# Kernel optimization log

Hardware: AMD Instinct MI355X
Metric: run time of the kernel (lower is better)

## Reference

```python
import jax, jax.numpy as jnp
import numpy as np


def setup_inputs() -> dict:
    key = jax.random.key(0)
    ks = jax.random.split(key, 9)
    B, T, D, H = 64, 512, 512, 512
    inp = {
        "x": jax.random.normal(ks[0], (B, T, D), dtype=jnp.float32),
        "W_c": jax.random.normal(ks[1], (D, H), dtype=jnp.float32) * 0.02,
        "W_i": jax.random.normal(ks[2], (D, H), dtype=jnp.float32) * 0.02,
        "W_f": jax.random.normal(ks[3], (D, H), dtype=jnp.float32) * 0.02,
        "W_o": jax.random.normal(ks[4], (D, H), dtype=jnp.float32) * 0.02,
        "U_c": jax.random.normal(ks[5], (H, H), dtype=jnp.float32) * 0.02,
        "U_i": jax.random.normal(ks[6], (H, H), dtype=jnp.float32) * 0.02,
        "U_f": jax.random.normal(ks[7], (H, H), dtype=jnp.float32) * 0.02,
        "U_o": jax.random.normal(ks[8], (H, H), dtype=jnp.float32) * 0.02,
        "b_c": jnp.zeros((H,), dtype=jnp.float32),
        "b_i": jnp.zeros((H,), dtype=jnp.float32),
        "b_f": jnp.zeros((H,), dtype=jnp.float32),
        "b_o": jnp.zeros((H,), dtype=jnp.float32),
    }
    return inp


def reference(x, W_c, W_i, W_f, W_o, U_c, U_i, U_f, U_o, b_c, b_i, b_f, b_o):
    # x: [B, T, D] -> scan over time-major [T, B, D]
    B, T, D = x.shape
    H = W_c.shape[1]
    h0 = jnp.zeros((B, H), dtype=x.dtype)
    c0 = jnp.zeros((B, H), dtype=x.dtype)

    # Precompute input projections for all timesteps (same math, hoisted
    # out of the recurrence since x does not depend on state).
    xt = jnp.transpose(x, (1, 0, 2))  # [T, B, D]
    xa = jnp.einsum('tbd,dh->tbh', xt, W_c) + b_c
    xi = jnp.einsum('tbd,dh->tbh', xt, W_i) + b_i
    xf = jnp.einsum('tbd,dh->tbh', xt, W_f) + b_f
    xo = jnp.einsum('tbd,dh->tbh', xt, W_o) + b_o

    def step(carry, elems):
        h, c = carry
        xa_t, xi_t, xf_t, xo_t = elems
        a = jnp.tanh(xa_t + h @ U_c)
        i = jax.nn.sigmoid(xi_t + h @ U_i)
        f = jax.nn.sigmoid(xf_t + h @ U_f)
        o = jax.nn.sigmoid(xo_t + h @ U_o)
        c_new = i * a + f * c
        h_new = o * jnp.tanh(c_new)
        return (h_new, c_new), h_new

    _, hs = jax.lax.scan(step, (h0, c0), (xa, xi, xf, xo))  # hs: [T, B, H]
    return jnp.transpose(hs, (1, 0, 2))  # return_sequence=True -> [B, T, H]
```

## Files before the change

### kernel.cpp

```cpp
#include <hip/hip_runtime.h>
#include <cstdint>
#include <cstddef>

typedef _Float16 half8  __attribute__((ext_vector_type(8)));
typedef _Float16 half2v __attribute__((ext_vector_type(2)));
typedef float    floatx4 __attribute__((ext_vector_type(4)));

#define B_  64
#define T_  512
#define D_  512
#define H_  512
#define NG  2048

#if defined(__has_builtin)
#if __has_builtin(__builtin_amdgcn_fdot2)
#define HAVE_FDOT2 1
#endif
#endif

static __device__ __forceinline__ float fdot2_acc(half2v a, half2v b, float c) {
#ifdef HAVE_FDOT2
  return __builtin_amdgcn_fdot2(a, b, c, false);
#else
  return fmaf((float)a[0], (float)b[0], fmaf((float)a[1], (float)b[1], c));
#endif
}
static __device__ __forceinline__ half2v h2(half8 v, int i) {
  half2v r; r[0] = v[2*i]; r[1] = v[2*i+1]; return r;
}
static __device__ __forceinline__ float fast_sigmoid(float x) {
  return 1.0f / (1.0f + __expf(-x));
}
static __device__ __forceinline__ float fast_tanh(float x) {
  x = fminf(15.0f, fmaxf(-15.0f, x));
  float e = __expf(2.0f * x);
  return (e - 1.0f) / (e + 1.0f);
}

#define LDS_BARRIER() do {                                   \
    asm volatile("s_waitcnt lgkmcnt(0)" ::: "memory");       \
    __builtin_amdgcn_s_barrier();                            \
  } while (0)

__global__ __launch_bounds__(256) void proj_kernel(
    const float* __restrict__ x,
    const float* __restrict__ Wc, const float* __restrict__ Wi,
    const float* __restrict__ Wf, const float* __restrict__ Wo,
    const float* __restrict__ bc, const float* __restrict__ bi,
    const float* __restrict__ bf2, const float* __restrict__ bo,
    _Float16* __restrict__ XG)
{
  const int tiles_n = NG / 64;
  int tM = blockIdx.x / tiles_n;
  int tN = blockIdx.x % tiles_n;
  int r0 = tM * 64;
  int t0 = r0 >> 6;
  int n0 = tN * 64;
  int g  = n0 >> 9;
  const float* W    = (g==0) ? Wc : (g==1) ? Wi : (g==2) ? Wf : Wo;
  const float* bias = (g==0) ? bc : (g==1) ? bi : (g==2) ? bf2 : bo;
  int j0 = n0 & (H_-1);

  __shared__ _Float16 Al[64*40];
  __shared__ _Float16 Bl[64*40];

  int tid  = threadIdx.x;
  int wave = tid >> 6;
  int lane = tid & 63;

  floatx4 acc[4] = {};

  int arow = tid >> 2;
  int ak0  = (tid & 3) * 8;
  const float* xsrc = x + ((size_t)arow * T_ + t0) * D_;

  int bcol = tid & 63;
  int bk0  = (tid >> 6) * 8;

  for (int k0 = 0; k0 < D_; k0 += 32) {
    half8 av;
    #pragma unroll
    for (int i = 0; i < 8; ++i) av[i] = (_Float16)xsrc[k0 + ak0 + i];
    *(half8*)&Al[arow*40 + ak0] = av;

    half8 bv;
    #pragma unroll
    for (int i = 0; i < 8; ++i)
      bv[i] = (_Float16)W[(size_t)(k0 + bk0 + i) * H_ + j0 + bcol];
    *(half8*)&Bl[bcol*40 + bk0] = bv;

    __syncthreads();

    half8 afrag = *(half8*)&Al[(wave*16 + (lane & 15))*40 + (lane >> 4)*8];
    #pragma unroll
    for (int ct = 0; ct < 4; ++ct) {
      half8 bfrag = *(half8*)&Bl[(ct*16 + (lane & 15))*40 + (lane >> 4)*8];
      acc[ct] = __builtin_amdgcn_mfma_f32_16x16x32_f16(afrag, bfrag, acc[ct], 0, 0, 0);
    }
    __syncthreads();
  }

  #pragma unroll
  for (int ct = 0; ct < 4; ++ct) {
    int col = n0 + ct*16 + (lane & 15);
    float bvs = bias[col & (H_-1)];
    #pragma unroll
    for (int i = 0; i < 4; ++i) {
      int row = r0 + wave*16 + (lane >> 4)*4 + i;
      XG[(size_t)row * NG + col] = (_Float16)(acc[ct][i] + bvs);
    }
  }
}

#define SH 520

__global__ __launch_bounds__(256) void scan_kernel(
    const _Float16* __restrict__ XG,
    const float* __restrict__ Uc, const float* __restrict__ Ui,
    const float* __restrict__ Uf, const float* __restrict__ Uo,
    float* __restrict__ out, unsigned* __restrict__ dbuf)
{
  extern __shared__ _Float16 lds[];
  _Float16* U_lds = lds;
  _Float16* h_lds = lds + 64*SH;
  float*  act_buf = (float*)(lds + 72*SH);

  int tid = threadIdx.x;
  int grp = blockIdx.x & 7;
  int member = blockIdx.x >> 3;
  int j0 = member * 16;

  {
    int jj = tid & 15;
    int kk = tid >> 4;
    #pragma unroll
    for (int g = 0; g < 4; ++g) {
      const float* U = (g==0) ? Uc : (g==1) ? Ui : (g==2) ? Uf : Uo;
      _Float16* dst = &U_lds[(g*16 + jj)*SH];
      for (int k = kk; k < H_; k += 16)
        dst[k] = (_Float16)U[(size_t)k * H_ + j0 + jj];
    }
  }
  __syncthreads();

  int gh    = tid >> 7;
  int local = tid & 127;
  int b     = local >> 4;
  int jj    = local & 15;
  int bglob = grp*8 + b;
  int j = j0 + jj;

  const half8* Ur0 = (const half8*)&U_lds[((gh    )*16 + jj)*SH];
  const half8* Ur1 = (const half8*)&U_lds[((gh + 2)*16 + jj)*SH];
  const half8* Hr  = (const half8*)&h_lds[b*SH];

  int cb  = tid & 7;
  int cj0 = (tid >> 3) * 16;

  float c_reg = 0.0f;

  float xg0, xg1;
  {
    size_t xb = (size_t)bglob * NG;
    xg0 = (float)XG[xb + (size_t)gh*H_ + j];
    xg1 = (float)XG[xb + (size_t)(gh + 2)*H_ + j];
  }

  for (int t = 0; t < T_; ++t) {
    {
      const unsigned long long* src8 = (const unsigned long long*)dbuf
          + ((unsigned)(t & 1))*16384u + (unsigned)grp*2048u + (unsigned)tid*8u;
      unsigned long long want2 = (unsigned long long)((unsigned)t & 0xFFFFu);
      want2 |= want2 << 32;
      unsigned long long w8[8];
      unsigned pend = 0xFFu;
      for (;;) {
        #pragma unroll
        for (int q = 0; q < 8; ++q)
          if (pend & (1u << q))
            w8[q] = __hip_atomic_load(src8 + q, __ATOMIC_RELAXED,
                                      __HIP_MEMORY_SCOPE_AGENT);
        unsigned npend = 0;
        #pragma unroll
        for (int q = 0; q < 8; ++q)
          if ((pend & (1u << q)) &&
              ((w8[q] ^ want2) & 0x0000FFFF0000FFFFull))
            npend |= 1u << q;
        if (!npend) break;
        pend = npend;
        __builtin_amdgcn_s_sleep(2);
      }
      half8 hv0, hv1;
      #pragma unroll
      for (int q = 0; q < 4; ++q) {
        hv0[2*q]   = __builtin_bit_cast(_Float16, (unsigned short)(w8[q]   >> 16));
        hv0[2*q+1] = __builtin_bit_cast(_Float16, (unsigned short)(w8[q]   >> 48));
        hv1[2*q]   = __builtin_bit_cast(_Float16, (unsigned short)(w8[4+q] >> 16));
        hv1[2*q+1] = __builtin_bit_cast(_Float16, (unsigned short)(w8[4+q] >> 48));
      }
      *(half8*)&h_lds[cb*SH + cj0]     = hv0;
      *(half8*)&h_lds[cb*SH + cj0 + 8] = hv1;
    }
    LDS_BARRIER();

    float acc0 = 0.f, acc1 = 0.f;
    #pragma unroll 4
    for (int k8 = 0; k8 < H_/8; ++k8) {
      half8 hv = Hr[k8];
      half8 u0 = Ur0[k8];
      half8 u1 = Ur1[k8];
      #pragma unroll
      for (int i = 0; i < 4; ++i) {
        acc0 = fdot2_acc(h2(hv,i), h2(u0,i), acc0);
        acc1 = fdot2_acc(h2(hv,i), h2(u1,i), acc1);
      }
    }
    float pre0 = acc0 + xg0;
    float pre1 = acc1 + xg1;

    float act0 = (gh == 0) ? fast_tanh(pre0) : fast_sigmoid(pre0);
    float act1 = fast_sigmoid(pre1);

    if (gh == 1) {
      act_buf[local*2    ] = act0;
      act_buf[local*2 + 1] = act1;
    }
    LDS_BARRIER();

    if (gh == 0) {
      float iv = act_buf[local*2];
      float ov = act_buf[local*2 + 1];
      float cn = fmaf(act1, c_reg, iv * act0);
      c_reg = cn;
      float hval = ov * fast_tanh(cn);
      if (t + 1 < T_) {
        unsigned wv = ((unsigned)__builtin_bit_cast(unsigned short, (_Float16)hval) << 16)
                    | ((unsigned)(t + 1) & 0xFFFFu);
        unsigned idx = ((unsigned)((t + 1) & 1))*32768u + (unsigned)grp*4096u
                     + (unsigned)member*128u + (unsigned)local;
        __hip_atomic_store(&dbuf[idx], wv,
                           __ATOMIC_RELAXED, __HIP_MEMORY_SCOPE_AGENT);
      }
      out[((size_t)bglob * T_ + t) * H_ + j] = hval;
    }

    if (t + 1 < T_) {
      size_t xbn = ((size_t)(t + 1) * B_ + bglob) * NG;
      xg0 = (float)XG[xbn + (size_t)gh*H_ + j];
      xg1 = (float)XG[xbn + (size_t)(gh + 2)*H_ + j];
    }
  }
}

extern "C" void kernel_launch(void* const* d_in, const int* in_sizes, int n_in,
                              void* d_out, int out_size, void* d_ws, size_t ws_size,
                              hipStream_t stream)
{
  const float* x  = (const float*)d_in[0];
  const float* Wc = (const float*)d_in[1];
  const float* Wi = (const float*)d_in[2];
  const float* Wf = (const float*)d_in[3];
  const float* Wo = (const float*)d_in[4];
  const float* Uc = (const float*)d_in[5];
  const float* Ui = (const float*)d_in[6];
  const float* Uf = (const float*)d_in[7];
  const float* Uo = (const float*)d_in[8];
  const float* bc = (const float*)d_in[9];
  const float* bi = (const float*)d_in[10];
  const float* bf2= (const float*)d_in[11];
  const float* bo = (const float*)d_in[12];
  float* out = (float*)d_out;

  const size_t XG_BYTES = (size_t)T_ * B_ * NG * sizeof(_Float16);
  const size_t DB_BYTES = (size_t)2 * 8 * 4096 * sizeof(unsigned);

  if (ws_size < XG_BYTES + DB_BYTES) return;

  _Float16* XG   = (_Float16*)d_ws;
  unsigned* dbuf = (unsigned*)((char*)d_ws + XG_BYTES);

  (void)hipMemsetAsync(dbuf, 0, DB_BYTES, stream);

  proj_kernel<<<dim3((T_*B_/64) * (NG/64)), dim3(256), 0, stream>>>(
      x, Wc, Wi, Wf, Wo, bc, bi, bf2, bo, XG);

  const int lds_bytes = 72*SH*2 + 256*4;
  (void)hipFuncSetAttribute(reinterpret_cast<const void*>(scan_kernel),
                      hipFuncAttributeMaxDynamicSharedMemorySize, lds_bytes);
  scan_kernel<<<dim3(256), dim3(256), lds_bytes, stream>>>(
      XG, Uc, Ui, Uf, Uo, out, dbuf);
}
```

Measured before the change: 2.372 ms.

## Poll h exchange with vector sc0 loads, falling back to atomic buffer

Each step's hidden-state values are now written to two buffers: a plain volatile store to a fast buffer and an agent-scope atomic store to a true buffer. Waiting workgroups poll the fast buffer with four wide global_load_dwordx4 sc0 loads, and every fourth sweep fall back to atomic loads from the true buffer so progress is guaranteed if cached data goes stale. The goal is to cut the latency of the cross-workgroup spin-wait that dominates the sequential scan. The cost is an extra store per element, twice the workspace, and reliance on sc0 load coherence behaviour.

```diff
diff --git a/kernel.cpp b/kernel.cpp
--- a/kernel.cpp
+++ b/kernel.cpp
@@ -5,6 +5,7 @@
 typedef _Float16 half8  __attribute__((ext_vector_type(8)));
 typedef _Float16 half2v __attribute__((ext_vector_type(2)));
 typedef float    floatx4 __attribute__((ext_vector_type(4)));
+typedef unsigned uint4v  __attribute__((ext_vector_type(4)));
 
 #define B_  64
 #define T_  512
@@ -118,7 +119,8 @@
     const _Float16* __restrict__ XG,
     const float* __restrict__ Uc, const float* __restrict__ Ui,
     const float* __restrict__ Uf, const float* __restrict__ Uo,
-    float* __restrict__ out, unsigned* __restrict__ dbuf)
+    float* __restrict__ out,
+    unsigned* __restrict__ fast_buf, unsigned* __restrict__ true_buf)
 {
   extern __shared__ _Float16 lds[];
   _Float16* U_lds = lds;
@@ -168,35 +170,58 @@
 
   for (int t = 0; t < T_; ++t) {
     {
-      const unsigned long long* src8 = (const unsigned long long*)dbuf
-          + ((unsigned)(t & 1))*16384u + (unsigned)grp*2048u + (unsigned)tid*8u;
-      unsigned long long want2 = (unsigned long long)((unsigned)t & 0xFFFFu);
-      want2 |= want2 << 32;
-      unsigned long long w8[8];
-      unsigned pend = 0xFFu;
+      unsigned base = ((unsigned)(t & 1))*32768u + (unsigned)grp*4096u
+                    + (unsigned)tid*16u;
+      const unsigned* fsrc = fast_buf + base;
+      const unsigned long long* tq = (const unsigned long long*)(true_buf + base);
+      unsigned want = (unsigned)t & 0xFFFFu;
+
+      unsigned w[16];
+      int sweep = 0;
       for (;;) {
+        if ((sweep & 3) == 3) {
+          unsigned long long q8[8];
+          #pragma unroll
+          for (int q = 0; q < 8; ++q)
+            q8[q] = __hip_atomic_load(tq + q, __ATOMIC_RELAXED,
+                                      __HIP_MEMORY_SCOPE_AGENT);
+          #pragma unroll
+          for (int q = 0; q < 8; ++q) {
+            w[2*q]   = (unsigned)q8[q];
+            w[2*q+1] = (unsigned)(q8[q] >> 32);
+          }
+        } else {
+          uint4v va, vb, vc, vd;
+          asm volatile(
+            "global_load_dwordx4 %0, %4, off sc0\n\t"
+            "global_load_dwordx4 %1, %4, off offset:16 sc0\n\t"
+            "global_load_dwordx4 %2, %4, off offset:32 sc0\n\t"
+            "global_load_dwordx4 %3, %4, off offset:48 sc0\n\t"
+            "s_waitcnt vmcnt(0)"
+            : "=&v"(va), "=&v"(vb), "=&v"(vc), "=&v"(vd)
+            : "v"(fsrc)
+            : "memory");
+          __builtin_amdgcn_sched_barrier(0);
+          #pragma unroll
+          for (int i = 0; i < 4; ++i) {
+            w[i]    = va[i];
+            w[4+i]  = vb[i];
+            w[8+i]  = vc[i];
+            w[12+i] = vd[i];
+          }
+        }
+        unsigned diff = 0;
         #pragma unroll
-        for (int q = 0; q < 8; ++q)
-          if (pend & (1u << q))
-            w8[q] = __hip_atomic_load(src8 + q, __ATOMIC_RELAXED,
-                                      __HIP_MEMORY_SCOPE_AGENT);
-        unsigned npend = 0;
-        #pragma unroll
-        for (int q = 0; q < 8; ++q)
-          if ((pend & (1u << q)) &&
-              ((w8[q] ^ want2) & 0x0000FFFF0000FFFFull))
-            npend |= 1u << q;
-        if (!npend) break;
-        pend = npend;
-        __builtin_amdgcn_s_sleep(2);
+        for (int i = 0; i < 16; ++i) diff |= (w[i] ^ want) & 0xFFFFu;
+        if (!diff) break;
+        __builtin_amdgcn_s_sleep(1);
+        ++sweep;
       }
       half8 hv0, hv1;
       #pragma unroll
-      for (int q = 0; q < 4; ++q) {
-        hv0[2*q]   = __builtin_bit_cast(_Float16, (unsigned short)(w8[q]   >> 16));
-        hv0[2*q+1] = __builtin_bit_cast(_Float16, (unsigned short)(w8[q]   >> 48));
-        hv1[2*q]   = __builtin_bit_cast(_Float16, (unsigned short)(w8[4+q] >> 16));
-        hv1[2*q+1] = __builtin_bit_cast(_Float16, (unsigned short)(w8[4+q] >> 48));
+      for (int i = 0; i < 8; ++i) {
+        hv0[i] = __builtin_bit_cast(_Float16, (unsigned short)(w[i]   >> 16));
+        hv1[i] = __builtin_bit_cast(_Float16, (unsigned short)(w[8+i] >> 16));
       }
       *(half8*)&h_lds[cb*SH + cj0]     = hv0;
       *(half8*)&h_lds[cb*SH + cj0 + 8] = hv1;
@@ -238,7 +263,8 @@
                     | ((unsigned)(t + 1) & 0xFFFFu);
         unsigned idx = ((unsigned)((t + 1) & 1))*32768u + (unsigned)grp*4096u
                      + (unsigned)member*128u + (unsigned)local;
-        __hip_atomic_store(&dbuf[idx], wv,
+        *(volatile unsigned*)&fast_buf[idx] = wv;
+        __hip_atomic_store(&true_buf[idx], wv,
                            __ATOMIC_RELAXED, __HIP_MEMORY_SCOPE_AGENT);
       }
       out[((size_t)bglob * T_ + t) * H_ + j] = hval;
@@ -271,15 +297,16 @@
   const float* bo = (const float*)d_in[12];
   float* out = (float*)d_out;
 
-  const size_t XG_BYTES = (size_t)T_ * B_ * NG * sizeof(_Float16);
-  const size_t DB_BYTES = (size_t)2 * 8 * 4096 * sizeof(unsigned);
-
-  if (ws_size < XG_BYTES + DB_BYTES) return;
-
-  _Float16* XG   = (_Float16*)d_ws;
-  unsigned* dbuf = (unsigned*)((char*)d_ws + XG_BYTES);
-
-  (void)hipMemsetAsync(dbuf, 0, DB_BYTES, stream);
+  const size_t XG_BYTES  = (size_t)T_ * B_ * NG * sizeof(_Float16);
+  const size_t BUF_BYTES = (size_t)2 * 8 * 4096 * sizeof(unsigned);
+
+  if (ws_size < XG_BYTES + 2*BUF_BYTES) return;
+
+  _Float16* XG       = (_Float16*)d_ws;
+  unsigned* fast_buf = (unsigned*)((char*)d_ws + XG_BYTES);
+  unsigned* true_buf = (unsigned*)((char*)d_ws + XG_BYTES + BUF_BYTES);
+
+  (void)hipMemsetAsync(fast_buf, 0, 2*BUF_BYTES, stream);
 
   proj_kernel<<<dim3((T_*B_/64) * (NG/64)), dim3(256), 0, stream>>>(
       x, Wc, Wi, Wf, Wo, bc, bi, bf2, bo, XG);
@@ -288,5 +315,5 @@
   (void)hipFuncSetAttribute(reinterpret_cast<const void*>(scan_kernel),
                       hipFuncAttributeMaxDynamicSharedMemorySize, lds_bytes);
   scan_kernel<<<dim3(256), dim3(256), lds_bytes, stream>>>(
-      XG, Uc, Ui, Uf, Uo, out, dbuf);
-}
+      XG, Uc, Ui, Uf, Uo, out, fast_buf, true_buf);
+}
```

New measurement: 3.550 ms. 1.5x slower.

## Split scan batch into two half-steps with wave-local gate exchange

Applied to the files above, without the earlier changes.

Restructures the recurrent scan so each wave holds all four gates for 16 hidden units of one batch row, and exchanges the gate activations with cross-lane shuffles instead of an LDS buffer and an extra barrier. The U slice is stored in LDS in an interleaved k-major layout so a wave reads it with contiguous half8 loads. The 8 batch rows of a group are processed in two halves with separate double-buffered flag/h arrays. The idea is that the first half's h can be published and consumed while the second half is still being computed, overlapping the inter-block spin-wait with compute. The cost is two polling rounds and two LDS barriers per timestep, plus a more complex dbuf indexing scheme.

```diff
diff --git a/kernel.cpp b/kernel.cpp
--- a/kernel.cpp
+++ b/kernel.cpp
@@ -112,8 +112,6 @@
   }
 }
 
-#define SH 520
-
 __global__ __launch_bounds__(256) void scan_kernel(
     const _Float16* __restrict__ XG,
     const float* __restrict__ Uc, const float* __restrict__ Ui,
@@ -121,9 +119,8 @@
     float* __restrict__ out, unsigned* __restrict__ dbuf)
 {
   extern __shared__ _Float16 lds[];
-  _Float16* U_lds = lds;
-  _Float16* h_lds = lds + 64*SH;
-  float*  act_buf = (float*)(lds + 72*SH);
+  _Float16* U2    = lds;
+  _Float16* h_lds = lds + 32768;
 
   int tid = threadIdx.x;
   int grp = blockIdx.x & 7;
@@ -136,118 +133,118 @@
     #pragma unroll
     for (int g = 0; g < 4; ++g) {
       const float* U = (g==0) ? Uc : (g==1) ? Ui : (g==2) ? Uf : Uo;
-      _Float16* dst = &U_lds[(g*16 + jj)*SH];
       for (int k = kk; k < H_; k += 16)
-        dst[k] = (_Float16)U[(size_t)k * H_ + j0 + jj];
+        U2[((size_t)(k >> 3)*64 + g*16 + jj)*8 + (k & 7)] =
+            (_Float16)U[(size_t)k * H_ + j0 + jj];
     }
   }
   __syncthreads();
 
-  int gh    = tid >> 7;
-  int local = tid & 127;
-  int b     = local >> 4;
-  int jj    = local & 15;
-  int bglob = grp*8 + b;
-  int j = j0 + jj;
-
-  const half8* Ur0 = (const half8*)&U_lds[((gh    )*16 + jj)*SH];
-  const half8* Ur1 = (const half8*)&U_lds[((gh + 2)*16 + jj)*SH];
-  const half8* Hr  = (const half8*)&h_lds[b*SH];
-
-  int cb  = tid & 7;
-  int cj0 = (tid >> 3) * 16;
-
-  float c_reg = 0.0f;
-
-  float xg0, xg1;
+  int lane = tid & 63;
+  int wb   = tid >> 6;
+  int g    = lane >> 4;
+  int jj   = lane & 15;
+  int j    = j0 + jj;
+  bool isg0 = (g == 0);
+
+  int cb   = tid >> 6;
+  int col0 = (tid & 63) * 8;
+
+  int bgA = grp*8 + wb;
+  int bgB = grp*8 + 4 + wb;
+
+  float cA = 0.0f, cB = 0.0f;
+  float xgA, xgB;
   {
-    size_t xb = (size_t)bglob * NG;
-    xg0 = (float)XG[xb + (size_t)gh*H_ + j];
-    xg1 = (float)XG[xb + (size_t)(gh + 2)*H_ + j];
-  }
+    xgA = (float)XG[((size_t)bgA) * NG + (size_t)g*H_ + j];
+    xgB = (float)XG[((size_t)bgB) * NG + (size_t)g*H_ + j];
+  }
+
+  const half8* hrowA = (const half8*)&h_lds[0    + wb*512];
+  const half8* hrowB = (const half8*)&h_lds[2048 + wb*512];
+  const half8* urow  = (const half8*)U2;
 
   for (int t = 0; t < T_; ++t) {
-    {
-      const unsigned long long* src8 = (const unsigned long long*)dbuf
-          + ((unsigned)(t & 1))*16384u + (unsigned)grp*2048u + (unsigned)tid*8u;
-      unsigned long long want2 = (unsigned long long)((unsigned)t & 0xFFFFu);
-      want2 |= want2 << 32;
-      unsigned long long w8[8];
-      unsigned pend = 0xFFu;
-      for (;;) {
+    unsigned want = (unsigned)t & 0xFFFFu;
+    unsigned long long want2 = (unsigned long long)want * 0x0000000100000001ull;
+
+    #pragma unroll
+    for (int s = 0; s < 2; ++s) {
+      {
+        unsigned base = ((unsigned)(s*2 + (t & 1))*8u + (unsigned)grp)*2048u
+                      + (unsigned)tid*8u;
+        const unsigned long long* src4 = (const unsigned long long*)(dbuf + base);
+        unsigned long long w4[4];
+        unsigned pend = 0xFu;
+        for (;;) {
+          #pragma unroll
+          for (int q = 0; q < 4; ++q)
+            if (pend & (1u << q))
+              w4[q] = __hip_atomic_load(src4 + q, __ATOMIC_RELAXED,
+                                        __HIP_MEMORY_SCOPE_AGENT);
+          unsigned npend = 0;
+          #pragma unroll
+          for (int q = 0; q < 4; ++q)
+            if ((pend & (1u << q)) &&
+                ((w4[q] ^ want2) & 0x0000FFFF0000FFFFull))
+              npend |= 1u << q;
+          if (!npend) break;
+          pend = npend;
+          __builtin_amdgcn_s_sleep(1);
+        }
+        half8 hv;
         #pragma unroll
-        for (int q = 0; q < 8; ++q)
-          if (pend & (1u << q))
-            w8[q] = __hip_atomic_load(src8 + q, __ATOMIC_RELAXED,
-                                      __HIP_MEMORY_SCOPE_AGENT);
-        unsigned npend = 0;
+        for (int q = 0; q < 4; ++q) {
+          hv[2*q]   = __builtin_bit_cast(_Float16, (unsigned short)(w4[q] >> 16));
+          hv[2*q+1] = __builtin_bit_cast(_Float16, (unsigned short)(w4[q] >> 48));
+        }
+        *(half8*)&h_lds[s*2048 + cb*512 + col0] = hv;
+      }
+      LDS_BARRIER();
+
+      int bglob = (s == 0) ? bgA : bgB;
+      float xg  = (s == 0) ? xgA : xgB;
+
+      float xgn = 0.f;
+      if (t + 1 < T_)
+        xgn = (float)XG[((size_t)(t + 1)*B_ + bglob) * NG + (size_t)g*H_ + j];
+
+      const half8* hrow = (s == 0) ? hrowA : hrowB;
+      float acc = 0.f;
+      #pragma unroll 8
+      for (int k8 = 0; k8 < 64; ++k8) {
+        half8 hv8 = hrow[k8];
+        half8 uv8 = urow[k8*64 + lane];
         #pragma unroll
-        for (int q = 0; q < 8; ++q)
-          if ((pend & (1u << q)) &&
-              ((w8[q] ^ want2) & 0x0000FFFF0000FFFFull))
-            npend |= 1u << q;
-        if (!npend) break;
-        pend = npend;
-        __builtin_amdgcn_s_sleep(2);
+        for (int i = 0; i < 4; ++i)
+          acc = fdot2_acc(h2(hv8, i), h2(uv8, i), acc);
       }
-      half8 hv0, hv1;
-      #pragma unroll
-      for (int q = 0; q < 4; ++q) {
-        hv0[2*q]   = __builtin_bit_cast(_Float16, (unsigned short)(w8[q]   >> 16));
-        hv0[2*q+1] = __builtin_bit_cast(_Float16, (unsigned short)(w8[q]   >> 48));
-        hv1[2*q]   = __builtin_bit_cast(_Float16, (unsigned short)(w8[4+q] >> 16));
-        hv1[2*q+1] = __builtin_bit_cast(_Float16, (unsigned short)(w8[4+q] >> 48));
+      float pre = acc + xg;
+
+      float act = isg0 ? fast_tanh(pre) : fast_sigmoid(pre);
+      float t16 = __shfl_xor(act, 16);
+      float ia  = act * t16;
+      float fv  = __shfl_xor(act, 32);
+      float ov  = __shfl_xor(t16, 32);
+
+      if (isg0) {
+        float c_old = (s == 0) ? cA : cB;
+        float cn = fmaf(fv, c_old, ia);
+        if (s == 0) cA = cn; else cB = cn;
+        float hval = ov * fast_tanh(cn);
+        if (t + 1 < T_) {
+          unsigned wv = ((unsigned)__builtin_bit_cast(unsigned short,
+                              (_Float16)hval) << 16)
+                      | ((unsigned)(t + 1) & 0xFFFFu);
+          unsigned pidx = ((unsigned)(s*2 + ((t + 1) & 1))*8u + (unsigned)grp)*2048u
+                        + (unsigned)(wb*512) + (unsigned)j;
+          __hip_atomic_store(&dbuf[pidx], wv,
+                             __ATOMIC_RELAXED, __HIP_MEMORY_SCOPE_AGENT);
+        }
+        out[((size_t)bglob * T_ + t) * H_ + j] = hval;
       }
-      *(half8*)&h_lds[cb*SH + cj0]     = hv0;
-      *(half8*)&h_lds[cb*SH + cj0 + 8] = hv1;
-    }
-    LDS_BARRIER();
-
-    float acc0 = 0.f, acc1 = 0.f;
-    #pragma unroll 4
-    for (int k8 = 0; k8 < H_/8; ++k8) {
-      half8 hv = Hr[k8];
-      half8 u0 = Ur0[k8];
-      half8 u1 = Ur1[k8];
-      #pragma unroll
-      for (int i = 0; i < 4; ++i) {
-        acc0 = fdot2_acc(h2(hv,i), h2(u0,i), acc0);
-        acc1 = fdot2_acc(h2(hv,i), h2(u1,i), acc1);
-      }
-    }
-    float pre0 = acc0 + xg0;
-    float pre1 = acc1 + xg1;
-
-    float act0 = (gh == 0) ? fast_tanh(pre0) : fast_sigmoid(pre0);
-    float act1 = fast_sigmoid(pre1);
-
-    if (gh == 1) {
-      act_buf[local*2    ] = act0;
-      act_buf[local*2 + 1] = act1;
-    }
-    LDS_BARRIER();
-
-    if (gh == 0) {
-      float iv = act_buf[local*2];
-      float ov = act_buf[local*2 + 1];
-      float cn = fmaf(act1, c_reg, iv * act0);
-      c_reg = cn;
-      float hval = ov * fast_tanh(cn);
-      if (t + 1 < T_) {
-        unsigned wv = ((unsigned)__builtin_bit_cast(unsigned short, (_Float16)hval) << 16)
-                    | ((unsigned)(t + 1) & 0xFFFFu);
-        unsigned idx = ((unsigned)((t + 1) & 1))*32768u + (unsigned)grp*4096u
-                     + (unsigned)member*128u + (unsigned)local;
-        __hip_atomic_store(&dbuf[idx], wv,
-                           __ATOMIC_RELAXED, __HIP_MEMORY_SCOPE_AGENT);
-      }
-      out[((size_t)bglob * T_ + t) * H_ + j] = hval;
-    }
-
-    if (t + 1 < T_) {
-      size_t xbn = ((size_t)(t + 1) * B_ + bglob) * NG;
-      xg0 = (float)XG[xbn + (size_t)gh*H_ + j];
-      xg1 = (float)XG[xbn + (size_t)(gh + 2)*H_ + j];
+
+      if (s == 0) xgA = xgn; else xgB = xgn;
     }
   }
 }
@@ -272,7 +269,7 @@
   float* out = (float*)d_out;
 
   const size_t XG_BYTES = (size_t)T_ * B_ * NG * sizeof(_Float16);
-  const size_t DB_BYTES = (size_t)2 * 8 * 4096 * sizeof(unsigned);
+  const size_t DB_BYTES = (size_t)2 * 2 * 8 * 2048 * sizeof(unsigned);
 
   if (ws_size < XG_BYTES + DB_BYTES) return;
 
@@ -284,7 +281,7 @@
   proj_kernel<<<dim3((T_*B_/64) * (NG/64)), dim3(256), 0, stream>>>(
       x, Wc, Wi, Wf, Wo, bc, bi, bf2, bo, XG);
 
-  const int lds_bytes = 72*SH*2 + 256*4;
+  const int lds_bytes = (32768 + 2*2048) * (int)sizeof(_Float16);
   (void)hipFuncSetAttribute(reinterpret_cast<const void*>(scan_kernel),
                       hipFuncAttributeMaxDynamicSharedMemorySize, lds_bytes);
   scan_kernel<<<dim3(256), dim3(256), lds_bytes, stream>>>(
```

Result: slower. 2.754 ms (+16.1%).

## Use MFMA with register-resident U fragments in persistent LSTM scan

Applied to the files above, without the earlier changes.

Replaces the per-thread fdot2 recurrent matvec with 16x16x32 MFMA instructions. The U weights now stay in registers as B fragments instead of in LDS, and h is staged into an LDS tile laid out for the A operand, padded with unused batch rows. Gates are interleaved across adjacent lanes and combined through shuffles, which removes the second LDS barrier and the act_buf exchange. This cuts LDS traffic and per-step latency in the serial recurrence, at the cost of wasted MFMA rows (only 8 of 16 batch rows are real) and higher register pressure.

```diff
diff --git a/kernel.cpp b/kernel.cpp
--- a/kernel.cpp
+++ b/kernel.cpp
@@ -3,8 +3,8 @@
 #include <cstddef>
 
 typedef _Float16 half8  __attribute__((ext_vector_type(8)));
-typedef _Float16 half2v __attribute__((ext_vector_type(2)));
 typedef float    floatx4 __attribute__((ext_vector_type(4)));
+typedef unsigned long long ull;
 
 #define B_  64
 #define T_  512
@@ -12,22 +12,6 @@
 #define H_  512
 #define NG  2048
 
-#if defined(__has_builtin)
-#if __has_builtin(__builtin_amdgcn_fdot2)
-#define HAVE_FDOT2 1
-#endif
-#endif
-
-static __device__ __forceinline__ float fdot2_acc(half2v a, half2v b, float c) {
-#ifdef HAVE_FDOT2
-  return __builtin_amdgcn_fdot2(a, b, c, false);
-#else
-  return fmaf((float)a[0], (float)b[0], fmaf((float)a[1], (float)b[1], c));
-#endif
-}
-static __device__ __forceinline__ half2v h2(half8 v, int i) {
-  half2v r; r[0] = v[2*i]; r[1] = v[2*i+1]; return r;
-}
 static __device__ __forceinline__ float fast_sigmoid(float x) {
   return 1.0f / (1.0f + __expf(-x));
 }
@@ -41,6 +25,8 @@
     asm volatile("s_waitcnt lgkmcnt(0)" ::: "memory");       \
     __builtin_amdgcn_s_barrier();                            \
   } while (0)
+
+#define TAGMASK 0x0000FFFF0000FFFFull
 
 __global__ __launch_bounds__(256) void proj_kernel(
     const float* __restrict__ x,
@@ -112,67 +98,60 @@
   }
 }
 
-#define SH 520
-
 __global__ __launch_bounds__(256) void scan_kernel(
     const _Float16* __restrict__ XG,
     const float* __restrict__ Uc, const float* __restrict__ Ui,
     const float* __restrict__ Uf, const float* __restrict__ Uo,
     float* __restrict__ out, unsigned* __restrict__ dbuf)
 {
-  extern __shared__ _Float16 lds[];
-  _Float16* U_lds = lds;
-  _Float16* h_lds = lds + 64*SH;
-  float*  act_buf = (float*)(lds + 72*SH);
+  __shared__ _Float16 h_lds[16*512];
 
   int tid = threadIdx.x;
   int grp = blockIdx.x & 7;
   int member = blockIdx.x >> 3;
-  int j0 = member * 16;
-
-  {
-    int jj = tid & 15;
-    int kk = tid >> 4;
-    #pragma unroll
-    for (int g = 0; g < 4; ++g) {
-      const float* U = (g==0) ? Uc : (g==1) ? Ui : (g==2) ? Uf : Uo;
-      _Float16* dst = &U_lds[(g*16 + jj)*SH];
-      for (int k = kk; k < H_; k += 16)
-        dst[k] = (_Float16)U[(size_t)k * H_ + j0 + jj];
-    }
-  }
-  __syncthreads();
-
-  int gh    = tid >> 7;
-  int local = tid & 127;
-  int b     = local >> 4;
-  int jj    = local & 15;
-  int bglob = grp*8 + b;
-  int j = j0 + jj;
-
-  const half8* Ur0 = (const half8*)&U_lds[((gh    )*16 + jj)*SH];
-  const half8* Ur1 = (const half8*)&U_lds[((gh + 2)*16 + jj)*SH];
-  const half8* Hr  = (const half8*)&h_lds[b*SH];
-
-  int cb  = tid & 7;
-  int cj0 = (tid >> 3) * 16;
-
-  float c_reg = 0.0f;
-
-  float xg0, xg1;
-  {
-    size_t xb = (size_t)bglob * NG;
-    xg0 = (float)XG[xb + (size_t)gh*H_ + j];
-    xg1 = (float)XG[xb + (size_t)(gh + 2)*H_ + j];
-  }
+
+  int lane = tid & 63;
+  int w    = tid >> 6;
+  int c16  = lane & 15;
+  int sub  = lane >> 4;
+  int g    = c16 & 3;
+  int jjl  = c16 >> 2;
+  int jcol = member*16 + w*4 + jjl;
+  int hi   = sub;
+  bool pub = (g == 0) && (hi < 2);
+
+  const float* Ug = (g==0) ? Uc : (g==1) ? Ui : (g==2) ? Uf : Uo;
+  half8 uf[16];
+  #pragma unroll
+  for (int ks = 0; ks < 16; ++ks) {
+    half8 v;
+    #pragma unroll
+    for (int q = 0; q < 8; ++q)
+      v[q] = (_Float16)Ug[(size_t)(ks*32 + sub*8 + q) * H_ + jcol];
+    uf[ks] = v;
+  }
+
+  int sm  = tid >> 3;
+  int sb  = tid & 7;
+  _Float16* stg = &h_lds[(sm >> 1)*512 + sb*32 + (sm & 1)*16];
+
+  const _Float16* abase = &h_lds[c16*32 + sub*8];
+
+  floatx4 c4 = {0.f, 0.f, 0.f, 0.f};
+  float xg[4] = {0.f, 0.f, 0.f, 0.f};
+  #pragma unroll
+  for (int i = 0; i < 4; ++i)
+    if (hi < 2)
+      xg[i] = (float)XG[(size_t)(grp*8 + hi*4 + i) * NG + g*512 + jcol];
 
   for (int t = 0; t < T_; ++t) {
+    LDS_BARRIER();
+
     {
-      const unsigned long long* src8 = (const unsigned long long*)dbuf
-          + ((unsigned)(t & 1))*16384u + (unsigned)grp*2048u + (unsigned)tid*8u;
-      unsigned long long want2 = (unsigned long long)((unsigned)t & 0xFFFFu);
-      want2 |= want2 << 32;
-      unsigned long long w8[8];
+      const ull* src8 = (const ull*)dbuf
+          + ((size_t)(t & 1))*16384u + (size_t)grp*2048u + (size_t)tid*8u;
+      ull want2 = (ull)(unsigned)(t & 0xFFFF) * 0x0000000100000001ull;
+      ull w8[8];
       unsigned pend = 0xFFu;
       for (;;) {
         #pragma unroll
@@ -183,8 +162,7 @@
         unsigned npend = 0;
         #pragma unroll
         for (int q = 0; q < 8; ++q)
-          if ((pend & (1u << q)) &&
-              ((w8[q] ^ want2) & 0x0000FFFF0000FFFFull))
+          if ((pend & (1u << q)) && ((w8[q] ^ want2) & TAGMASK))
             npend |= 1u << q;
         if (!npend) break;
         pend = npend;
@@ -193,61 +171,64 @@
       half8 hv0, hv1;
       #pragma unroll
       for (int q = 0; q < 4; ++q) {
-        hv0[2*q]   = __builtin_bit_cast(_Float16, (unsigned short)(w8[q]   >> 16));
+        hv0[2*q]   = __builtin_bit_cast(_Float16, (unsigned short)((unsigned)w8[q]   >> 16));
         hv0[2*q+1] = __builtin_bit_cast(_Float16, (unsigned short)(w8[q]   >> 48));
-        hv1[2*q]   = __builtin_bit_cast(_Float16, (unsigned short)(w8[4+q] >> 16));
+        hv1[2*q]   = __builtin_bit_cast(_Float16, (unsigned short)((unsigned)w8[4+q] >> 16));
         hv1[2*q+1] = __builtin_bit_cast(_Float16, (unsigned short)(w8[4+q] >> 48));
       }
-      *(half8*)&h_lds[cb*SH + cj0]     = hv0;
-      *(half8*)&h_lds[cb*SH + cj0 + 8] = hv1;
+      *(half8*)stg       = hv0;
+      *(half8*)(stg + 8) = hv1;
     }
     LDS_BARRIER();
 
-    float acc0 = 0.f, acc1 = 0.f;
-    #pragma unroll 4
-    for (int k8 = 0; k8 < H_/8; ++k8) {
-      half8 hv = Hr[k8];
-      half8 u0 = Ur0[k8];
-      half8 u1 = Ur1[k8];
+    floatx4 a0 = {0.f,0.f,0.f,0.f}, a1 = {0.f,0.f,0.f,0.f};
+    #pragma unroll
+    for (int ks = 0; ks < 16; ks += 2) {
+      half8 af0 = *(const half8*)(abase + ks*512);
+      a0 = __builtin_amdgcn_mfma_f32_16x16x32_f16(af0, uf[ks],   a0, 0, 0, 0);
+      half8 af1 = *(const half8*)(abase + (ks+1)*512);
+      a1 = __builtin_amdgcn_mfma_f32_16x16x32_f16(af1, uf[ks+1], a1, 0, 0, 0);
+    }
+
+    float hval[4];
+    #pragma unroll
+    for (int i = 0; i < 4; ++i) {
+      float pre = (a0[i] + a1[i]) + xg[i];
+      float act = (g == 0) ? fast_tanh(pre) : fast_sigmoid(pre);
+      float t1  = __shfl_xor(act, 1);
+      float ia  = act * t1;
+      float fv  = __shfl_xor(act, 2);
+      float ov  = __shfl_xor(t1, 2);
+      float cn  = fmaf(fv, c4[i], ia);
+      c4[i] = cn;
+      hval[i] = ov * fast_tanh(cn);
+    }
+
+    if (pub) {
+      if (t + 1 < T_) {
+        #pragma unroll
+        for (int i = 0; i < 4; ++i) {
+          unsigned wv = ((unsigned)__builtin_bit_cast(unsigned short,
+                              (_Float16)hval[i]) << 16)
+                      | ((unsigned)(t + 1) & 0xFFFFu);
+          unsigned widx = ((unsigned)((t + 1) & 1))*32768u + (unsigned)grp*4096u
+                        + (unsigned)member*128u
+                        + (unsigned)((hi*4 + i)*16 + w*4 + jjl);
+          __hip_atomic_store(&dbuf[widx], wv,
+                             __ATOMIC_RELAXED, __HIP_MEMORY_SCOPE_AGENT);
+        }
+      }
       #pragma unroll
-      for (int i = 0; i < 4; ++i) {
-        acc0 = fdot2_acc(h2(hv,i), h2(u0,i), acc0);
-        acc1 = fdot2_acc(h2(hv,i), h2(u1,i), acc1);
-      }
-    }
-    float pre0 = acc0 + xg0;
-    float pre1 = acc1 + xg1;
-
-    float act0 = (gh == 0) ? fast_tanh(pre0) : fast_sigmoid(pre0);
-    float act1 = fast_sigmoid(pre1);
-
-    if (gh == 1) {
-      act_buf[local*2    ] = act0;
-      act_buf[local*2 + 1] = act1;
-    }
-    LDS_BARRIER();
-
-    if (gh == 0) {
-      float iv = act_buf[local*2];
-      float ov = act_buf[local*2 + 1];
-      float cn = fmaf(act1, c_reg, iv * act0);
-      c_reg = cn;
-      float hval = ov * fast_tanh(cn);
-      if (t + 1 < T_) {
-        unsigned wv = ((unsigned)__builtin_bit_cast(unsigned short, (_Float16)hval) << 16)
-                    | ((unsigned)(t + 1) & 0xFFFFu);
-        unsigned idx = ((unsigned)((t + 1) & 1))*32768u + (unsigned)grp*4096u
-                     + (unsigned)member*128u + (unsigned)local;
-        __hip_atomic_store(&dbuf[idx], wv,
-                           __ATOMIC_RELAXED, __HIP_MEMORY_SCOPE_AGENT);
-      }
-      out[((size_t)bglob * T_ + t) * H_ + j] = hval;
+      for (int i = 0; i < 4; ++i)
+        out[((size_t)(grp*8 + hi*4 + i) * T_ + t) * H_ + jcol] = hval[i];
     }
 
     if (t + 1 < T_) {
-      size_t xbn = ((size_t)(t + 1) * B_ + bglob) * NG;
-      xg0 = (float)XG[xbn + (size_t)gh*H_ + j];
-      xg1 = (float)XG[xbn + (size_t)(gh + 2)*H_ + j];
+      #pragma unroll
+      for (int i = 0; i < 4; ++i)
+        if (hi < 2)
+          xg[i] = (float)XG[((size_t)(t + 1)*B_ + grp*8 + hi*4 + i) * NG
+                            + g*512 + jcol];
     }
   }
 }
@@ -284,9 +265,6 @@
   proj_kernel<<<dim3((T_*B_/64) * (NG/64)), dim3(256), 0, stream>>>(
       x, Wc, Wi, Wf, Wo, bc, bi, bf2, bo, XG);
 
-  const int lds_bytes = 72*SH*2 + 256*4;
-  (void)hipFuncSetAttribute(reinterpret_cast<const void*>(scan_kernel),
-                      hipFuncAttributeMaxDynamicSharedMemorySize, lds_bytes);
-  scan_kernel<<<dim3(256), dim3(256), lds_bytes, stream>>>(
+  scan_kernel<<<dim3(256), dim3(256), 0, stream>>>(
       XG, Uc, Ui, Uf, Uo, out, dbuf);
 }
```

Measured after the change: 2.060 ms. -13.2%, faster.
